# Kernel optimization log

Hardware: AMD Instinct MI355X
Metric: run time of the kernel (lower is better)

Reference implementation:

```python
import jax, jax.numpy as jnp
import numpy as np

D = 256      # d_model
H = 8        # num heads
HD = D // H  # head dim
DFF = 1024   # feedforward dim
S = 1024     # seq len
B = 8        # batch
EPS = 1e-5


def _layernorm(x, g, b):
    mu = jnp.mean(x, axis=-1, keepdims=True)
    var = jnp.mean((x - mu) ** 2, axis=-1, keepdims=True)
    return (x - mu) * jax.lax.rsqrt(var + EPS) * g + b


def setup_inputs() -> dict:
    key = jax.random.key(0)
    ks = jax.random.split(key, 12)
    xav = lambda k, shape: jax.random.uniform(
        k, shape, jnp.float32, -1.0, 1.0) * np.sqrt(6.0 / (shape[0] + shape[-1]))
    return {
        "src": jax.random.normal(ks[0], (S, B, D), jnp.float32),
        "bias": jax.random.normal(ks[1], (B, H, S, S), jnp.float32),
        "in_proj_w": xav(ks[2], (3 * D, D)),
        "in_proj_b": jnp.zeros((3 * D,), jnp.float32),
        "out_w": xav(ks[3], (D, D)),
        "out_b": jnp.zeros((D,), jnp.float32),
        "w1": xav(ks[4], (DFF, D)),
        "b1": jnp.zeros((DFF,), jnp.float32),
        "w2": xav(ks[5], (D, DFF)),
        "b2": jnp.zeros((D,), jnp.float32),
        "g1": jnp.ones((D,), jnp.float32),
        "be1": jnp.zeros((D,), jnp.float32),
        "g2": jnp.ones((D,), jnp.float32),
        "be2": jnp.zeros((D,), jnp.float32),
    }


def reference(src, bias, in_proj_w, in_proj_b, out_w, out_b,
              w1, b1, w2, b2, g1, be1, g2, be2):
    # Pre-norm (note: residual uses the NORMED src, matching the torch code)
    x = _layernorm(src, g1, be1)                       # [S,B,D]
    qkv = x @ in_proj_w.T + in_proj_b                  # [S,B,3D]
    q, k, v = jnp.split(qkv, 3, axis=-1)
    q = q * (HD ** -0.5)
    # [S,B,D] -> [B,H,S,HD]
    to_heads = lambda t: t.reshape(S, B, H, HD).transpose(1, 2, 0, 3)
    qh, kh, vh = to_heads(q), to_heads(k), to_heads(v)
    scores = jnp.einsum('bhsd,bhtd->bhst', qh, kh) + bias
    attn = jax.nn.softmax(scores, axis=-1)             # [B,H,S,S]
    ctx = jnp.einsum('bhst,bhtd->bhsd', attn, vh)      # [B,H,S,HD]
    ctx = ctx.transpose(2, 0, 1, 3).reshape(S, B, D)
    attn_out = ctx @ out_w.T + out_b
    x = x + attn_out                                   # residual (eval: no dropout)
    y = _layernorm(x, g2, be2)
    ff = jax.nn.relu(y @ w1.T + b1) @ w2.T + b2
    return y + ff
```

## Files before the change

kernel.cpp:

```cpp
#include <hip/hip_runtime.h>
#include <hip/hip_bf16.h>
#include <cstdint>

typedef unsigned short u16;
typedef __attribute__((ext_vector_type(8))) short bf16x8;
typedef __attribute__((ext_vector_type(4))) float f32x4;

#define S_LEN 1024
#define BATCH 8
#define DMODEL 256
#define NHEAD 8
#define HDIM 32
#define DFF 1024
#define NROWS (S_LEN * BATCH)

static __device__ __forceinline__ u16 f2b(float f) {
    union { float f; unsigned u; } x{f};
    unsigned r = (x.u + 0x7fffu + ((x.u >> 16) & 1u)) >> 16;
    return (u16)r;
}

__global__ __launch_bounds__(256) void prep_kernel(
    const float* __restrict__ in, const float* __restrict__ g1,
    const float* __restrict__ be1, float* __restrict__ of, u16* __restrict__ ob,
    const float* __restrict__ ipw, const float* __restrict__ outw,
    const float* __restrict__ w1, const float* __restrict__ w2,
    const float* __restrict__ ipb,
    u16* __restrict__ wqkv, u16* __restrict__ wout,
    u16* __restrict__ w1b, u16* __restrict__ w2b, float* __restrict__ bq)
{
    const float s = 0.17677669529663689f;
    if (blockIdx.x >= 2048) {
        const int i4 = ((int)blockIdx.x - 2048) * 1024 + threadIdx.x * 4;
        const float* src; u16* dst; int off; float sc = 1.0f;
        if (i4 < 196608)      { src = ipw;  dst = wqkv; off = 0;      if (i4 < 65536) sc = s; }
        else if (i4 < 262144) { src = outw; dst = wout; off = 196608; }
        else if (i4 < 524288) { src = w1;   dst = w1b;  off = 262144; }
        else                  { src = w2;   dst = w2b;  off = 524288; }
        const float4 v = *(const float4*)(src + i4 - off);
        uint2 pk;
        pk.x = (unsigned)f2b(v.x * sc) | ((unsigned)f2b(v.y * sc) << 16);
        pk.y = (unsigned)f2b(v.z * sc) | ((unsigned)f2b(v.w * sc) << 16);
        *(uint2*)(dst + i4 - off) = pk;
        if (i4 < 768) {
            const float4 b = *(const float4*)(ipb + i4);
            const float bs = (i4 < 256) ? s : 1.0f;
            *(float4*)(bq + i4) = make_float4(b.x * bs, b.y * bs, b.z * bs, b.w * bs);
        }
        return;
    }
    const int w = threadIdx.x >> 6, l = threadIdx.x & 63;
    const int row = blockIdx.x * 4 + w;
    const float4 v = *(const float4*)(in + (size_t)row * DMODEL + l * 4);
    float s0 = v.x + v.y + v.z + v.w;
    #pragma unroll
    for (int o = 32; o; o >>= 1) s0 += __shfl_xor(s0, o);
    const float mu = s0 * (1.0f / DMODEL);
    const float dx = v.x - mu, dy = v.y - mu, dz = v.z - mu, dw = v.w - mu;
    float sq = dx * dx + dy * dy + dz * dz + dw * dw;
    #pragma unroll
    for (int o = 32; o; o >>= 1) sq += __shfl_xor(sq, o);
    const float rs = rsqrtf(sq * (1.0f / DMODEL) + 1e-5f);
    const float4 gv = *(const float4*)(g1 + l * 4);
    const float4 bv = *(const float4*)(be1 + l * 4);
    const float r0 = dx * rs * gv.x + bv.x;
    const float r1 = dy * rs * gv.y + bv.y;
    const float r2 = dz * rs * gv.z + bv.z;
    const float r3 = dw * rs * gv.w + bv.w;
    *(float4*)(of + (size_t)row * DMODEL + l * 4) = make_float4(r0, r1, r2, r3);
    uint2 pk;
    pk.x = (unsigned)f2b(r0) | ((unsigned)f2b(r1) << 16);
    pk.y = (unsigned)f2b(r2) | ((unsigned)f2b(r3) << 16);
    *(uint2*)(ob + (size_t)row * DMODEL + l * 4) = pk;
}

template <int MF>
__device__ __forceinline__ void gemm_core(
    const u16* __restrict__ A, const u16* __restrict__ Bw,
    int N, int K, int nbase, int rowbase, u16* sB, f32x4 acc[MF][4])
{
    const int tid = threadIdx.x, w = tid >> 6, l = tid & 63;
    const int g = l >> 4, q = l & 15;
    const u16* Arow = A + (size_t)(rowbase + w * (MF * 16) + q) * K + g * 8;

    const int sbr = tid >> 3, sseg = tid & 7;
    const size_t bsrc0 = (size_t)(nbase + sbr) * K + sseg * 8;
    const size_t bsrc1 = (size_t)(nbase + sbr + 32) * K + sseg * 8;
    const int d0 = sbr * 128 + ((sseg * 16) ^ ((sbr & 7) << 4));
    const int d1 = d0 + 32 * 128;

    {
        const uint4 r0 = *(const uint4*)(Bw + bsrc0);
        const uint4 r1 = *(const uint4*)(Bw + bsrc1);
        *(uint4*)((char*)sB + d0) = r0;
        *(uint4*)((char*)sB + d1) = r1;
    }
    const int NC = K >> 6;
    for (int c = 0; c < NC; ++c) {
        __syncthreads();
        char* sBc = (char*)sB + (c & 1) * 8192;
        char* sBn = (char*)sB + ((c + 1) & 1) * 8192;
        uint4 p0, p1;
        if (c + 1 < NC) {
            p0 = *(const uint4*)(Bw + bsrc0 + (c + 1) * 64);
            p1 = *(const uint4*)(Bw + bsrc1 + (c + 1) * 64);
        }
        const int kk = c * 64;
        #pragma unroll
        for (int ks = 0; ks < 2; ++ks) {
            bf16x8 af[MF];
            #pragma unroll
            for (int m = 0; m < MF; ++m)
                af[m] = *(const bf16x8*)(Arow + (size_t)m * 16 * K + kk + ks * 32);
            #pragma unroll
            for (int n = 0; n < 4; ++n) {
                const int rr = n * 16 + q;
                const bf16x8 bf = *(const bf16x8*)(
                    sBc + rr * 128 + ((ks * 64 + g * 16) ^ ((rr & 7) << 4)));
                #pragma unroll
                for (int m = 0; m < MF; ++m)
                    acc[m][n] = __builtin_amdgcn_mfma_f32_16x16x32_bf16(bf, af[m], acc[m][n], 0, 0, 0);
            }
        }
        if (c + 1 < NC) {
            *(uint4*)(sBn + d0) = p0;
            *(uint4*)(sBn + d1) = p1;
        }
    }
}

__global__ __launch_bounds__(256) void gemm_qkv(
    const u16* __restrict__ A, const u16* __restrict__ Bw,
    const float* __restrict__ bias,
    u16* __restrict__ Qh, u16* __restrict__ Kh, u16* __restrict__ Vt)
{
    __shared__ u16 sB[2][64 * 64];
    const int tid = threadIdx.x, w = tid >> 6, l = tid & 63;
    const int g = l >> 4, q = l & 15;
    const int rowbase = blockIdx.x * 128, nbase = blockIdx.y * 64;
    f32x4 acc[2][4] = {};
    gemm_core<2>(A, Bw, 768, 256, nbase, rowbase, &sB[0][0], acc);

    #pragma unroll
    for (int m = 0; m < 2; ++m) {
        const int row = rowbase + w * 32 + m * 16 + q;
        const int s = row >> 3, b = row & 7;
        if (nbase < 512) {
            u16* dst = (nbase >= 256) ? Kh : Qh;
            #pragma unroll
            for (int n = 0; n < 4; ++n) {
                const int col = nbase + n * 16 + g * 4;
                const float4 bv = *(const float4*)(bias + col);
                const int cc = col & 255, h = cc >> 5, hd = cc & 31;
                const int bh = b * 8 + h;
                uint2 pk;
                pk.x = (unsigned)f2b(acc[m][n][0] + bv.x) | ((unsigned)f2b(acc[m][n][1] + bv.y) << 16);
                pk.y = (unsigned)f2b(acc[m][n][2] + bv.z) | ((unsigned)f2b(acc[m][n][3] + bv.w) << 16);
                *(uint2*)(dst + ((size_t)bh * S_LEN + s) * HDIM + hd) = pk;
            }
        } else {
            #pragma unroll
            for (int n = 0; n < 4; ++n) {
                const int col = nbase + n * 16 + g * 4;
                const float4 bv = *(const float4*)(bias + col);
                const int cc = col - 512, h = cc >> 5, hd = cc & 31;
                const int bh = b * 8 + h;
                Vt[((size_t)bh * HDIM + hd + 0) * S_LEN + s] = f2b(acc[m][n][0] + bv.x);
                Vt[((size_t)bh * HDIM + hd + 1) * S_LEN + s] = f2b(acc[m][n][1] + bv.y);
                Vt[((size_t)bh * HDIM + hd + 2) * S_LEN + s] = f2b(acc[m][n][2] + bv.z);
                Vt[((size_t)bh * HDIM + hd + 3) * S_LEN + s] = f2b(acc[m][n][3] + bv.w);
            }
        }
    }
}

__global__ __launch_bounds__(256) void attn_kernel(
    const u16* __restrict__ Qh, const u16* __restrict__ Kh,
    const u16* __restrict__ Vt, const float* __restrict__ bias,
    u16* __restrict__ ctx)
{
    __shared__ u16 sK[2][64 * 32];
    __shared__ u16 sV[2][32 * 64];
    __shared__ u16 sP[4][16 * 64];
    const int tid = threadIdx.x, w = tid >> 6, l = tid & 63;
    const int g = l >> 4, q = l & 15;
    const int bh = blockIdx.y, b = bh >> 3, h = bh & 7;
    const int qbase = blockIdx.x * 64 + w * 16;
    const int qrow = qbase + q;

    const bf16x8 qf = *(const bf16x8*)(Qh + ((size_t)bh * S_LEN + qrow) * HDIM + g * 8);
    const float* brow = bias + ((size_t)bh * S_LEN + qrow) * S_LEN;
    u16* Pw = sP[w];
    const int swz = (q & 7) << 4;

    const u16* KsrcBase = Kh + ((size_t)bh * S_LEN + w * 16 + q) * HDIM + g * 8;
    const u16* VsrcBase = Vt + ((size_t)bh * HDIM + (w & 1) * 16 + q) * S_LEN
                             + (w >> 1) * 32 + g * 8;
    u16* KdstA = &sK[0][tid * 8]; u16* KdstB = &sK[1][tid * 8];
    u16* VdstA = &sV[0][tid * 8]; u16* VdstB = &sV[1][tid * 8];

    f32x4 ctxa[2] = {{0,0,0,0},{0,0,0,0}};
    float m = -1e30f, lsum = 0.f;

    auto loadB = [&](int kt, f32x4* bv) {
        #pragma unroll
        for (int n = 0; n < 4; ++n)
            bv[n] = __builtin_nontemporal_load(
                (const f32x4*)(brow + kt * 64 + n * 16 + g * 4));
    };

    auto proc = [&](int buf, const f32x4* bv) {
        f32x4 sc[4];
        #pragma unroll
        for (int n = 0; n < 4; ++n) {
            const bf16x8 kf = *(const bf16x8*)(&sK[buf][(n * 64 + l) * 8]);
            f32x4 z = {0, 0, 0, 0};
            sc[n] = __builtin_amdgcn_mfma_f32_16x16x32_bf16(kf, qf, z, 0, 0, 0);
        }
        #pragma unroll
        for (int n = 0; n < 4; ++n)
            #pragma unroll
            for (int r = 0; r < 4; ++r) sc[n][r] += bv[n][r];

        float mx = sc[0][0];
        #pragma unroll
        for (int n = 0; n < 4; ++n)
            #pragma unroll
            for (int r = 0; r < 4; ++r) mx = fmaxf(mx, sc[n][r]);
        mx = fmaxf(mx, __shfl_xor(mx, 16));
        mx = fmaxf(mx, __shfl_xor(mx, 32));
        const float mn = fmaxf(m, mx);
        const float corr = __expf(m - mn);
        float su = 0.f;
        u16 pb[16];
        #pragma unroll
        for (int n = 0; n < 4; ++n)
            #pragma unroll
            for (int r = 0; r < 4; ++r) {
                const float pv = __expf(sc[n][r] - mn);
                su += pv;
                pb[n * 4 + r] = f2b(pv);
            }
        su += __shfl_xor(su, 16);
        su += __shfl_xor(su, 32);
        lsum = lsum * corr + su;
        m = mn;
        #pragma unroll
        for (int jg = 0; jg < 2; ++jg)
            #pragma unroll
            for (int r = 0; r < 4; ++r) ctxa[jg][r] *= corr;

        #pragma unroll
        for (int n = 0; n < 4; ++n) {
            uint2 pk;
            pk.x = (unsigned)pb[n * 4] | ((unsigned)pb[n * 4 + 1] << 16);
            pk.y = (unsigned)pb[n * 4 + 2] | ((unsigned)pb[n * 4 + 3] << 16);
            *(uint2*)((char*)Pw + q * 128 + ((n * 32 + g * 8) ^ swz)) = pk;
        }

        #pragma unroll
        for (int ks = 0; ks < 2; ++ks) {
            const bf16x8 pf = *(const bf16x8*)((char*)Pw + q * 128 + ((ks * 64 + g * 16) ^ swz));
            #pragma unroll
            for (int jg = 0; jg < 2; ++jg) {
                const bf16x8 vf = *(const bf16x8*)(&sV[buf][((ks * 2 + jg) * 64 + l) * 8]);
                ctxa[jg] = __builtin_amdgcn_mfma_f32_16x16x32_bf16(vf, pf, ctxa[jg], 0, 0, 0);
            }
        }
    };

    f32x4 bv0[4], bv1[4];
    {
        const uint4 kr = *(const uint4*)(KsrcBase);
        const uint4 vr = *(const uint4*)(VsrcBase);
        *(uint4*)KdstA = kr;
        *(uint4*)VdstA = vr;
        loadB(0, bv0);
    }
    __syncthreads();

    for (int kt = 0; kt < 16; kt += 2) {
        {
            uint4 kr, vr;
            kr = *(const uint4*)(KsrcBase + (size_t)(kt + 1) * 64 * HDIM);
            vr = *(const uint4*)(VsrcBase + (size_t)(kt + 1) * 64);
            loadB(kt + 1, bv1);
            proc(0, bv0);
            *(uint4*)KdstB = kr;
            *(uint4*)VdstB = vr;
        }
        __syncthreads();
        {
            uint4 kr, vr;
            if (kt + 2 < 16) {
                kr = *(const uint4*)(KsrcBase + (size_t)(kt + 2) * 64 * HDIM);
                vr = *(const uint4*)(VsrcBase + (size_t)(kt + 2) * 64);
                loadB(kt + 2, bv0);
            }
            proc(1, bv1);
            if (kt + 2 < 16) {
                *(uint4*)KdstA = kr;
                *(uint4*)VdstA = vr;
            }
        }
        __syncthreads();
    }

    const float inv = 1.0f / lsum;
    #pragma unroll
    for (int jg = 0; jg < 2; ++jg) {
        uint2 pk;
        pk.x = (unsigned)f2b(ctxa[jg][0] * inv) | ((unsigned)f2b(ctxa[jg][1] * inv) << 16);
        pk.y = (unsigned)f2b(ctxa[jg][2] * inv) | ((unsigned)f2b(ctxa[jg][3] * inv) << 16);
        *(uint2*)(ctx + ((size_t)qrow * 8 + b) * DMODEL + h * 32 + jg * 16 + g * 4) = pk;
    }
}

__global__ __launch_bounds__(256) void oproj_ln(
    const u16* __restrict__ ctx, const u16* __restrict__ wob,
    const float* __restrict__ ob, const float* __restrict__ xf,
    const float* __restrict__ g2, const float* __restrict__ be2,
    float* __restrict__ yf, u16* __restrict__ yb)
{
    __shared__ float s1[4][32], s2[4][32];
    const int tid = threadIdx.x, wv = tid >> 6, l = tid & 63;
    const int g = l >> 4, q = l & 15;
    const int rowbase = blockIdx.x * 32;
    f32x4 acc[2][4] = {};
    const u16* Arow = ctx + (size_t)(rowbase + q) * 256 + g * 8;
    const u16* Brow = wob + (size_t)(wv * 64 + q) * 256 + g * 8;

    #pragma unroll 2
    for (int kk = 0; kk < 256; kk += 32) {
        bf16x8 af[2];
        #pragma unroll
        for (int m = 0; m < 2; ++m)
            af[m] = *(const bf16x8*)(Arow + (size_t)m * 16 * 256 + kk);
        #pragma unroll
        for (int n = 0; n < 4; ++n) {
            const bf16x8 bf = *(const bf16x8*)(Brow + (size_t)n * 16 * 256 + kk);
            #pragma unroll
            for (int m = 0; m < 2; ++m)
                acc[m][n] = __builtin_amdgcn_mfma_f32_16x16x32_bf16(bf, af[m], acc[m][n], 0, 0, 0);
        }
    }

    float sum[2] = {0.f, 0.f};
    #pragma unroll
    for (int m = 0; m < 2; ++m) {
        const int row = rowbase + m * 16 + q;
        #pragma unroll
        for (int n = 0; n < 4; ++n) {
            const int col = wv * 64 + n * 16 + g * 4;
            const float4 bv = *(const float4*)(ob + col);
            const float4 rv = *(const float4*)(xf + (size_t)row * 256 + col);
            acc[m][n][0] += bv.x + rv.x; acc[m][n][1] += bv.y + rv.y;
            acc[m][n][2] += bv.z + rv.z; acc[m][n][3] += bv.w + rv.w;
            sum[m] += acc[m][n][0] + acc[m][n][1] + acc[m][n][2] + acc[m][n][3];
        }
        sum[m] += __shfl_xor(sum[m], 16);
        sum[m] += __shfl_xor(sum[m], 32);
    }
    if (l < 16) { s1[wv][q] = sum[0]; s1[wv][16 + q] = sum[1]; }
    __syncthreads();
    float mu[2], rs[2];
    #pragma unroll
    for (int m = 0; m < 2; ++m) {
        const int lr = m * 16 + q;
        mu[m] = (s1[0][lr] + s1[1][lr] + s1[2][lr] + s1[3][lr]) * (1.0f / 256);
    }
    float sq[2] = {0.f, 0.f};
    #pragma unroll
    for (int m = 0; m < 2; ++m) {
        #pragma unroll
        for (int n = 0; n < 4; ++n)
            #pragma unroll
            for (int r = 0; r < 4; ++r) {
                const float d = acc[m][n][r] - mu[m];
                sq[m] += d * d;
            }
        sq[m] += __shfl_xor(sq[m], 16);
        sq[m] += __shfl_xor(sq[m], 32);
    }
    if (l < 16) { s2[wv][q] = sq[0]; s2[wv][16 + q] = sq[1]; }
    __syncthreads();
    #pragma unroll
    for (int m = 0; m < 2; ++m) {
        const int lr = m * 16 + q;
        rs[m] = rsqrtf((s2[0][lr] + s2[1][lr] + s2[2][lr] + s2[3][lr]) * (1.0f / 256) + 1e-5f);
    }

    #pragma unroll
    for (int m = 0; m < 2; ++m) {
        const int row = rowbase + m * 16 + q;
        #pragma unroll
        for (int n = 0; n < 4; ++n) {
            const int col = wv * 64 + n * 16 + g * 4;
            const float4 gv = *(const float4*)(g2 + col);
            const float4 b2 = *(const float4*)(be2 + col);
            const float y0 = (acc[m][n][0] - mu[m]) * rs[m] * gv.x + b2.x;
            const float y1 = (acc[m][n][1] - mu[m]) * rs[m] * gv.y + b2.y;
            const float y2 = (acc[m][n][2] - mu[m]) * rs[m] * gv.z + b2.z;
            const float y3 = (acc[m][n][3] - mu[m]) * rs[m] * gv.w + b2.w;
            *(float4*)(yf + (size_t)row * 256 + col) = make_float4(y0, y1, y2, y3);
            uint2 pk;
            pk.x = (unsigned)f2b(y0) | ((unsigned)f2b(y1) << 16);
            pk.y = (unsigned)f2b(y2) | ((unsigned)f2b(y3) << 16);
            *(uint2*)(yb + (size_t)row * 256 + col) = pk;
        }
    }
}

__global__ __launch_bounds__(512) void ffn_fused(
    const u16* __restrict__ yb, const u16* __restrict__ w1b,
    const float* __restrict__ b1, const u16* __restrict__ w2b,
    const float* __restrict__ b2, const float* __restrict__ yf,
    float* __restrict__ out)
{
    __shared__ u16 sH[32 * 1024];
    const int tid = threadIdx.x, w = tid >> 6, l = tid & 63;
    const int g = l >> 4, q = l & 15;
    const int rowbase = blockIdx.x * 32;

    {
        const int cbase = w * 128;
        f32x4 acc[2][8] = {};
        const u16* Arow = yb + (size_t)(rowbase + q) * 256 + g * 8;
        const u16* Brow = w1b + (size_t)(cbase + q) * 256 + g * 8;
        #pragma unroll 2
        for (int kk = 0; kk < 256; kk += 32) {
            bf16x8 af[2];
            #pragma unroll
            for (int m = 0; m < 2; ++m)
                af[m] = *(const bf16x8*)(Arow + (size_t)m * 16 * 256 + kk);
            #pragma unroll
            for (int n = 0; n < 8; ++n) {
                const bf16x8 bf = *(const bf16x8*)(Brow + (size_t)n * 16 * 256 + kk);
                #pragma unroll
                for (int m = 0; m < 2; ++m)
                    acc[m][n] = __builtin_amdgcn_mfma_f32_16x16x32_bf16(bf, af[m], acc[m][n], 0, 0, 0);
            }
        }
        #pragma unroll
        for (int m = 0; m < 2; ++m) {
            const int lr = m * 16 + q;
            #pragma unroll
            for (int n = 0; n < 8; ++n) {
                const int col = cbase + n * 16 + g * 4;
                const float4 bv = *(const float4*)(b1 + col);
                const float v0 = fmaxf(acc[m][n][0] + bv.x, 0.f);
                const float v1 = fmaxf(acc[m][n][1] + bv.y, 0.f);
                const float v2 = fmaxf(acc[m][n][2] + bv.z, 0.f);
                const float v3 = fmaxf(acc[m][n][3] + bv.w, 0.f);
                uint2 pk;
                pk.x = (unsigned)f2b(v0) | ((unsigned)f2b(v1) << 16);
                pk.y = (unsigned)f2b(v2) | ((unsigned)f2b(v3) << 16);
                const int x = col * 2;
                const int sx = (x & ~127) | ((x & 127) ^ ((lr & 7) << 4));
                *(uint2*)((char*)sH + lr * 2048 + sx) = pk;
            }
        }
    }
    __syncthreads();

    {
        const int obase = w * 32;
        f32x4 acc[2][2] = {};
        const u16* Brow = w2b + (size_t)(obase + q) * 1024 + g * 8;
        for (int kk = 0; kk < 1024; kk += 32) {
            bf16x8 af[2];
            #pragma unroll
            for (int m = 0; m < 2; ++m) {
                const int lr = m * 16 + q;
                const int x = (kk + g * 8) * 2;
                const int sx = (x & ~127) | ((x & 127) ^ ((lr & 7) << 4));
                af[m] = *(const bf16x8*)((char*)sH + lr * 2048 + sx);
            }
            #pragma unroll
            for (int n = 0; n < 2; ++n) {
                const bf16x8 bf = *(const bf16x8*)(Brow + (size_t)n * 16 * 1024 + kk);
                #pragma unroll
                for (int m = 0; m < 2; ++m)
                    acc[m][n] = __builtin_amdgcn_mfma_f32_16x16x32_bf16(bf, af[m], acc[m][n], 0, 0, 0);
            }
        }
        #pragma unroll
        for (int m = 0; m < 2; ++m) {
            const int row = rowbase + m * 16 + q;
            #pragma unroll
            for (int n = 0; n < 2; ++n) {
                const int col = obase + n * 16 + g * 4;
                const float4 bv = *(const float4*)(b2 + col);
                const float4 rv = *(const float4*)(yf + (size_t)row * 256 + col);
                *(float4*)(out + (size_t)row * 256 + col) = make_float4(
                    acc[m][n][0] + bv.x + rv.x, acc[m][n][1] + bv.y + rv.y,
                    acc[m][n][2] + bv.z + rv.z, acc[m][n][3] + bv.w + rv.w);
            }
        }
    }
}

extern "C" void kernel_launch(void* const* d_in, const int* in_sizes, int n_in,
                              void* d_out, int out_size, void* d_ws, size_t ws_size,
                              hipStream_t stream)
{
    const float* src  = (const float*)d_in[0];
    const float* bias = (const float*)d_in[1];
    const float* ipw  = (const float*)d_in[2];
    const float* ipb  = (const float*)d_in[3];
    const float* outw = (const float*)d_in[4];
    const float* outb = (const float*)d_in[5];
    const float* w1   = (const float*)d_in[6];
    const float* b1   = (const float*)d_in[7];
    const float* w2   = (const float*)d_in[8];
    const float* b2   = (const float*)d_in[9];
    const float* g1   = (const float*)d_in[10];
    const float* be1  = (const float*)d_in[11];
    const float* g2   = (const float*)d_in[12];
    const float* be2  = (const float*)d_in[13];

    char* p = (char*)d_ws;
    auto alloc = [&](size_t bytes) -> void* {
        void* r = (void*)p;
        p += (bytes + 255) & ~(size_t)255;
        return r;
    };
    float* xf   = (float*)alloc((size_t)NROWS * DMODEL * 4);
    u16*   xb   = (u16*)  alloc((size_t)NROWS * DMODEL * 2);
    u16*   Qh   = (u16*)  alloc((size_t)64 * S_LEN * HDIM * 2);
    u16*   Kb   = (u16*)  alloc((size_t)64 * S_LEN * HDIM * 2);
    u16*   Vt   = (u16*)  alloc((size_t)64 * S_LEN * HDIM * 2);
    u16*   ctx  = (u16*)  alloc((size_t)NROWS * DMODEL * 2);
    float* yf   = (float*)alloc((size_t)NROWS * DMODEL * 4);
    u16*   yb   = (u16*)  alloc((size_t)NROWS * DMODEL * 2);
    u16*   wqkv = (u16*)  alloc((size_t)768 * 256 * 2);
    u16*   wob  = (u16*)  alloc((size_t)256 * 256 * 2);
    u16*   w1b  = (u16*)  alloc((size_t)1024 * 256 * 2);
    u16*   w2b  = (u16*)  alloc((size_t)256 * 1024 * 2);
    float* bq   = (float*)alloc(768 * 4);

    prep_kernel<<<2816, 256, 0, stream>>>(src, g1, be1, xf, xb,
                                          ipw, outw, w1, w2, ipb,
                                          wqkv, wob, w1b, w2b, bq);
    gemm_qkv<<<dim3(64, 12), 256, 0, stream>>>(xb, wqkv, bq, Qh, Kb, Vt);
    attn_kernel<<<dim3(16, 64), 256, 0, stream>>>(Qh, Kb, Vt, bias, ctx);
    oproj_ln<<<256, 256, 0, stream>>>(ctx, wob, outb, xf, g2, be2, yf, yb);
    ffn_fused<<<256, 512, 0, stream>>>(yb, w1b, b1, w2b, b2, yf, (float*)d_out);
}
```

Baseline: 158.9 us.

## Split fused FFN into two tiled LDS-staged GEMMs and widen QKV tile

```diff
diff --git a/kernel.cpp b/kernel.cpp
--- a/kernel.cpp
+++ b/kernel.cpp
@@ -74,36 +74,43 @@
     *(uint2*)(ob + (size_t)row * DMODEL + l * 4) = pk;
 }
 
-template <int MF>
+template <int MF, int NF>
 __device__ __forceinline__ void gemm_core(
     const u16* __restrict__ A, const u16* __restrict__ Bw,
-    int N, int K, int nbase, int rowbase, u16* sB, f32x4 acc[MF][4])
+    int K, int nbase, int rowbase, u16* sB, f32x4 acc[MF][NF])
 {
     const int tid = threadIdx.x, w = tid >> 6, l = tid & 63;
     const int g = l >> 4, q = l & 15;
     const u16* Arow = A + (size_t)(rowbase + w * (MF * 16) + q) * K + g * 8;
 
     const int sbr = tid >> 3, sseg = tid & 7;
-    const size_t bsrc0 = (size_t)(nbase + sbr) * K + sseg * 8;
-    const size_t bsrc1 = (size_t)(nbase + sbr + 32) * K + sseg * 8;
-    const int d0 = sbr * 128 + ((sseg * 16) ^ ((sbr & 7) << 4));
-    const int d1 = d0 + 32 * 128;
+    const int LOADS = NF / 2;
+    const int CHUNK = NF * 16 * 128;
+    size_t bsrc[LOADS];
+    int d[LOADS];
+    #pragma unroll
+    for (int i = 0; i < LOADS; ++i) {
+        bsrc[i] = (size_t)(nbase + sbr + 32 * i) * K + sseg * 8;
+        d[i] = (sbr + 32 * i) * 128 + ((sseg * 16) ^ ((sbr & 7) << 4));
+    }
 
     {
-        const uint4 r0 = *(const uint4*)(Bw + bsrc0);
-        const uint4 r1 = *(const uint4*)(Bw + bsrc1);
-        *(uint4*)((char*)sB + d0) = r0;
-        *(uint4*)((char*)sB + d1) = r1;
+        #pragma unroll
+        for (int i = 0; i < LOADS; ++i) {
+            const uint4 r = *(const uint4*)(Bw + bsrc[i]);
+            *(uint4*)((char*)sB + d[i]) = r;
+        }
     }
     const int NC = K >> 6;
     for (int c = 0; c < NC; ++c) {
         __syncthreads();
-        char* sBc = (char*)sB + (c & 1) * 8192;
-        char* sBn = (char*)sB + ((c + 1) & 1) * 8192;
-        uint4 p0, p1;
+        char* sBc = (char*)sB + (c & 1) * CHUNK;
+        char* sBn = (char*)sB + ((c + 1) & 1) * CHUNK;
+        uint4 p[LOADS];
         if (c + 1 < NC) {
-            p0 = *(const uint4*)(Bw + bsrc0 + (c + 1) * 64);
-            p1 = *(const uint4*)(Bw + bsrc1 + (c + 1) * 64);
+            #pragma unroll
+            for (int i = 0; i < LOADS; ++i)
+                p[i] = *(const uint4*)(Bw + bsrc[i] + (c + 1) * 64);
         }
         const int kk = c * 64;
         #pragma unroll
@@ -113,7 +120,7 @@
             for (int m = 0; m < MF; ++m)
                 af[m] = *(const bf16x8*)(Arow + (size_t)m * 16 * K + kk + ks * 32);
             #pragma unroll
-            for (int n = 0; n < 4; ++n) {
+            for (int n = 0; n < NF; ++n) {
                 const int rr = n * 16 + q;
                 const bf16x8 bf = *(const bf16x8*)(
                     sBc + rr * 128 + ((ks * 64 + g * 16) ^ ((rr & 7) << 4)));
@@ -123,8 +130,9 @@
             }
         }
         if (c + 1 < NC) {
-            *(uint4*)(sBn + d0) = p0;
-            *(uint4*)(sBn + d1) = p1;
+            #pragma unroll
+            for (int i = 0; i < LOADS; ++i)
+                *(uint4*)(sBn + d[i]) = p[i];
         }
     }
 }
@@ -134,35 +142,30 @@
     const float* __restrict__ bias,
     u16* __restrict__ Qh, u16* __restrict__ Kh, u16* __restrict__ Vt)
 {
-    __shared__ u16 sB[2][64 * 64];
+    __shared__ u16 sB[2][128 * 64];
     const int tid = threadIdx.x, w = tid >> 6, l = tid & 63;
     const int g = l >> 4, q = l & 15;
-    const int rowbase = blockIdx.x * 128, nbase = blockIdx.y * 64;
-    f32x4 acc[2][4] = {};
-    gemm_core<2>(A, Bw, 768, 256, nbase, rowbase, &sB[0][0], acc);
+    const int rowbase = blockIdx.x * 128, nbase = blockIdx.y * 128;
+    f32x4 acc[2][8] = {};
+    gemm_core<2, 8>(A, Bw, 256, nbase, rowbase, &sB[0][0], acc);
 
     #pragma unroll
     for (int m = 0; m < 2; ++m) {
         const int row = rowbase + w * 32 + m * 16 + q;
         const int s = row >> 3, b = row & 7;
-        if (nbase < 512) {
-            u16* dst = (nbase >= 256) ? Kh : Qh;
-            #pragma unroll
-            for (int n = 0; n < 4; ++n) {
-                const int col = nbase + n * 16 + g * 4;
-                const float4 bv = *(const float4*)(bias + col);
+        #pragma unroll
+        for (int n = 0; n < 8; ++n) {
+            const int col = nbase + n * 16 + g * 4;
+            const float4 bv = *(const float4*)(bias + col);
+            if (col < 512) {
+                u16* dst = (col >= 256) ? Kh : Qh;
                 const int cc = col & 255, h = cc >> 5, hd = cc & 31;
                 const int bh = b * 8 + h;
                 uint2 pk;
                 pk.x = (unsigned)f2b(acc[m][n][0] + bv.x) | ((unsigned)f2b(acc[m][n][1] + bv.y) << 16);
                 pk.y = (unsigned)f2b(acc[m][n][2] + bv.z) | ((unsigned)f2b(acc[m][n][3] + bv.w) << 16);
                 *(uint2*)(dst + ((size_t)bh * S_LEN + s) * HDIM + hd) = pk;
-            }
-        } else {
-            #pragma unroll
-            for (int n = 0; n < 4; ++n) {
-                const int col = nbase + n * 16 + g * 4;
-                const float4 bv = *(const float4*)(bias + col);
+            } else {
                 const int cc = col - 512, h = cc >> 5, hd = cc & 31;
                 const int bh = b * 8 + h;
                 Vt[((size_t)bh * HDIM + hd + 0) * S_LEN + s] = f2b(acc[m][n][0] + bv.x);
@@ -170,6 +173,63 @@
                 Vt[((size_t)bh * HDIM + hd + 2) * S_LEN + s] = f2b(acc[m][n][2] + bv.z);
                 Vt[((size_t)bh * HDIM + hd + 3) * S_LEN + s] = f2b(acc[m][n][3] + bv.w);
             }
+        }
+    }
+}
+
+__global__ __launch_bounds__(256) void gemm_ffn1(
+    const u16* __restrict__ A, const u16* __restrict__ Bw,
+    const float* __restrict__ bias, u16* __restrict__ outb)
+{
+    __shared__ u16 sB[2][128 * 64];
+    const int tid = threadIdx.x, w = tid >> 6, l = tid & 63;
+    const int g = l >> 4, q = l & 15;
+    const int rowbase = blockIdx.x * 128, nbase = blockIdx.y * 128;
+    f32x4 acc[2][8] = {};
+    gemm_core<2, 8>(A, Bw, 256, nbase, rowbase, &sB[0][0], acc);
+
+    #pragma unroll
+    for (int m = 0; m < 2; ++m) {
+        const int row = rowbase + w * 32 + m * 16 + q;
+        #pragma unroll
+        for (int n = 0; n < 8; ++n) {
+            const int col = nbase + n * 16 + g * 4;
+            const float4 bv = *(const float4*)(bias + col);
+            const float v0 = fmaxf(acc[m][n][0] + bv.x, 0.f);
+            const float v1 = fmaxf(acc[m][n][1] + bv.y, 0.f);
+            const float v2 = fmaxf(acc[m][n][2] + bv.z, 0.f);
+            const float v3 = fmaxf(acc[m][n][3] + bv.w, 0.f);
+            uint2 pk;
+            pk.x = (unsigned)f2b(v0) | ((unsigned)f2b(v1) << 16);
+            pk.y = (unsigned)f2b(v2) | ((unsigned)f2b(v3) << 16);
+            *(uint2*)(outb + (size_t)row * DFF + col) = pk;
+        }
+    }
+}
+
+__global__ __launch_bounds__(256) void gemm_ffn2(
+    const u16* __restrict__ A, const u16* __restrict__ Bw,
+    const float* __restrict__ bias, const float* __restrict__ resid,
+    float* __restrict__ outf)
+{
+    __shared__ u16 sB[2][64 * 64];
+    const int tid = threadIdx.x, w = tid >> 6, l = tid & 63;
+    const int g = l >> 4, q = l & 15;
+    const int rowbase = blockIdx.x * 128, nbase = blockIdx.y * 64;
+    f32x4 acc[2][4] = {};
+    gemm_core<2, 4>(A, Bw, 1024, nbase, rowbase, &sB[0][0], acc);
+
+    #pragma unroll
+    for (int m = 0; m < 2; ++m) {
+        const int row = rowbase + w * 32 + m * 16 + q;
+        #pragma unroll
+        for (int n = 0; n < 4; ++n) {
+            const int col = nbase + n * 16 + g * 4;
+            const float4 bv = *(const float4*)(bias + col);
+            const float4 rv = *(const float4*)(resid + (size_t)row * DMODEL + col);
+            *(float4*)(outf + (size_t)row * DMODEL + col) = make_float4(
+                acc[m][n][0] + bv.x + rv.x, acc[m][n][1] + bv.y + rv.y,
+                acc[m][n][2] + bv.z + rv.z, acc[m][n][3] + bv.w + rv.w);
         }
     }
 }
@@ -407,95 +467,6 @@
             pk.x = (unsigned)f2b(y0) | ((unsigned)f2b(y1) << 16);
             pk.y = (unsigned)f2b(y2) | ((unsigned)f2b(y3) << 16);
             *(uint2*)(yb + (size_t)row * 256 + col) = pk;
-        }
-    }
-}
-
-__global__ __launch_bounds__(512) void ffn_fused(
-    const u16* __restrict__ yb, const u16* __restrict__ w1b,
-    const float* __restrict__ b1, const u16* __restrict__ w2b,
-    const float* __restrict__ b2, const float* __restrict__ yf,
-    float* __restrict__ out)
-{
-    __shared__ u16 sH[32 * 1024];
-    const int tid = threadIdx.x, w = tid >> 6, l = tid & 63;
-    const int g = l >> 4, q = l & 15;
-    const int rowbase = blockIdx.x * 32;
-
-    {
-        const int cbase = w * 128;
-        f32x4 acc[2][8] = {};
-        const u16* Arow = yb + (size_t)(rowbase + q) * 256 + g * 8;
-        const u16* Brow = w1b + (size_t)(cbase + q) * 256 + g * 8;
-        #pragma unroll 2
-        for (int kk = 0; kk < 256; kk += 32) {
-            bf16x8 af[2];
-            #pragma unroll
-            for (int m = 0; m < 2; ++m)
-                af[m] = *(const bf16x8*)(Arow + (size_t)m * 16 * 256 + kk);
-            #pragma unroll
-            for (int n = 0; n < 8; ++n) {
-                const bf16x8 bf = *(const bf16x8*)(Brow + (size_t)n * 16 * 256 + kk);
-                #pragma unroll
-                for (int m = 0; m < 2; ++m)
-                    acc[m][n] = __builtin_amdgcn_mfma_f32_16x16x32_bf16(bf, af[m], acc[m][n], 0, 0, 0);
-            }
-        }
-        #pragma unroll
-        for (int m = 0; m < 2; ++m) {
-            const int lr = m * 16 + q;
-            #pragma unroll
-            for (int n = 0; n < 8; ++n) {
-                const int col = cbase + n * 16 + g * 4;
-                const float4 bv = *(const float4*)(b1 + col);
-                const float v0 = fmaxf(acc[m][n][0] + bv.x, 0.f);
-                const float v1 = fmaxf(acc[m][n][1] + bv.y, 0.f);
-                const float v2 = fmaxf(acc[m][n][2] + bv.z, 0.f);
-                const float v3 = fmaxf(acc[m][n][3] + bv.w, 0.f);
-                uint2 pk;
-                pk.x = (unsigned)f2b(v0) | ((unsigned)f2b(v1) << 16);
-                pk.y = (unsigned)f2b(v2) | ((unsigned)f2b(v3) << 16);
-                const int x = col * 2;
-                const int sx = (x & ~127) | ((x & 127) ^ ((lr & 7) << 4));
-                *(uint2*)((char*)sH + lr * 2048 + sx) = pk;
-            }
-        }
-    }
-    __syncthreads();
-
-    {
-        const int obase = w * 32;
-        f32x4 acc[2][2] = {};
-        const u16* Brow = w2b + (size_t)(obase + q) * 1024 + g * 8;
-        for (int kk = 0; kk < 1024; kk += 32) {
-            bf16x8 af[2];
-            #pragma unroll
-            for (int m = 0; m < 2; ++m) {
-                const int lr = m * 16 + q;
-                const int x = (kk + g * 8) * 2;
-                const int sx = (x & ~127) | ((x & 127) ^ ((lr & 7) << 4));
-                af[m] = *(const bf16x8*)((char*)sH + lr * 2048 + sx);
-            }
-            #pragma unroll
-            for (int n = 0; n < 2; ++n) {
-                const bf16x8 bf = *(const bf16x8*)(Brow + (size_t)n * 16 * 1024 + kk);
-                #pragma unroll
-                for (int m = 0; m < 2; ++m)
-                    acc[m][n] = __builtin_amdgcn_mfma_f32_16x16x32_bf16(bf, af[m], acc[m][n], 0, 0, 0);
-            }
-        }
-        #pragma unroll
-        for (int m = 0; m < 2; ++m) {
-            const int row = rowbase + m * 16 + q;
-            #pragma unroll
-            for (int n = 0; n < 2; ++n) {
-                const int col = obase + n * 16 + g * 4;
-                const float4 bv = *(const float4*)(b2 + col);
-                const float4 rv = *(const float4*)(yf + (size_t)row * 256 + col);
-                *(float4*)(out + (size_t)row * 256 + col) = make_float4(
-                    acc[m][n][0] + bv.x + rv.x, acc[m][n][1] + bv.y + rv.y,
-                    acc[m][n][2] + bv.z + rv.z, acc[m][n][3] + bv.w + rv.w);
-            }
         }
     }
 }
@@ -533,6 +504,7 @@
     u16*   ctx  = (u16*)  alloc((size_t)NROWS * DMODEL * 2);
     float* yf   = (float*)alloc((size_t)NROWS * DMODEL * 4);
     u16*   yb   = (u16*)  alloc((size_t)NROWS * DMODEL * 2);
+    u16*   hb   = (u16*)  alloc((size_t)NROWS * DFF * 2);
     u16*   wqkv = (u16*)  alloc((size_t)768 * 256 * 2);
     u16*   wob  = (u16*)  alloc((size_t)256 * 256 * 2);
     u16*   w1b  = (u16*)  alloc((size_t)1024 * 256 * 2);
@@ -542,8 +514,9 @@
     prep_kernel<<<2816, 256, 0, stream>>>(src, g1, be1, xf, xb,
                                           ipw, outw, w1, w2, ipb,
                                           wqkv, wob, w1b, w2b, bq);
-    gemm_qkv<<<dim3(64, 12), 256, 0, stream>>>(xb, wqkv, bq, Qh, Kb, Vt);
+    gemm_qkv<<<dim3(64, 6), 256, 0, stream>>>(xb, wqkv, bq, Qh, Kb, Vt);
     attn_kernel<<<dim3(16, 64), 256, 0, stream>>>(Qh, Kb, Vt, bias, ctx);
     oproj_ln<<<256, 256, 0, stream>>>(ctx, wob, outb, xf, g2, be2, yf, yb);
-    ffn_fused<<<256, 512, 0, stream>>>(yb, w1b, b1, w2b, b2, yf, (float*)d_out);
-}
+    gemm_ffn1<<<dim3(64, 8), 256, 0, stream>>>(yb, w1b, b1, hb);
+    gemm_ffn2<<<dim3(64, 4), 256, 0, stream>>>(hb, w2b, b2, yf, (float*)d_out);
+}
```

Result: no change. 157.3 us (-1.0%).
